# Optimization experiments

Measured on AMD Instinct MI355X. Metric: run time of the kernel, lower is better.

## Reference

```python
import jax, jax.numpy as jnp
import numpy as np

N_NODES = 100000
N_HEDGES = 20000
N_PAIRS = 1600000
D = 128


def setup_inputs() -> dict:
    key = jax.random.key(0)
    k1, k2, k3, k4, k5 = jax.random.split(key, 5)
    features = jax.random.normal(k1, (N_NODES, D), dtype=jnp.float32)
    W = jax.random.normal(k2, (D, D), dtype=jnp.float32) * (1.0 / np.sqrt(D))
    b = jax.random.normal(k3, (D,), dtype=jnp.float32) * 0.01
    node_idx = jax.random.randint(k4, (N_PAIRS,), 0, N_NODES, dtype=jnp.int32)
    hedge_idx = jax.random.randint(k5, (N_PAIRS,), 0, N_HEDGES, dtype=jnp.int32)
    return {"features": features, "W": W, "b": b,
            "node_idx": node_idx, "hedge_idx": hedge_idx, "n_hedges": N_HEDGES}


def reference(features, W, b, node_idx, hedge_idx, n_hedges):
    # features: [N, D]; (node_idx, hedge_idx): [E] incidence pairs
    N = features.shape[0]
    ones = jnp.ones(node_idx.shape, dtype=features.dtype)
    # node -> hyperedge mean (DGL copy_u + mean over 'in' etype)
    deg_e = jax.ops.segment_sum(ones, hedge_idx, num_segments=n_hedges)  # [He]
    h_edge = jax.ops.segment_sum(features[node_idx], hedge_idx, num_segments=n_hedges)
    h_edge = h_edge / jnp.maximum(deg_e, 1.0)[:, None]  # zero-degree edges -> 0
    # hyperedge -> node mean (copy_u + mean over 'contains' etype)
    deg_n = jax.ops.segment_sum(ones, node_idx, num_segments=N)  # [N]
    h_node = jax.ops.segment_sum(h_edge[hedge_idx], node_idx, num_segments=N)
    h_node = h_node / jnp.maximum(deg_n, 1.0)[:, None]
    # nn.Linear: x @ W.T + b
    return h_node @ W.T + b
```

## Files before the change

### kernel.cpp

```cpp
#include <hip/hip_runtime.h>

static constexpr int kD = 128;
static constexpr int kHedges = 20000;

static constexpr int kNCE = 157;
static constexpr int kCapCE = 11264;
static constexpr int kNCN = 196;
static constexpr int kCapCN = 9216;
static constexpr int kSliceE4 = 1664;
static constexpr int kSliceN4 = 1408;
static constexpr int kPmax = 1600;

__device__ __forceinline__ float u2f(unsigned u) { return __uint_as_float(u); }
__device__ __forceinline__ unsigned f2u(float f) { return __float_as_uint(f); }

__device__ __forceinline__ unsigned bfpack(float x, float y) {
  unsigned ux = f2u(x); ux = (ux + 0x7FFFu + ((ux >> 16) & 1u)) >> 16;
  unsigned uy = f2u(y); uy = (uy + 0x7FFFu + ((uy >> 16) & 1u)) & 0xFFFF0000u;
  return ux | uy;
}
__device__ __forceinline__ void bf8_acc(uint4 v, float* a) {
  a[0] += u2f(v.x << 16); a[1] += u2f(v.x & 0xFFFF0000u);
  a[2] += u2f(v.y << 16); a[3] += u2f(v.y & 0xFFFF0000u);
  a[4] += u2f(v.z << 16); a[5] += u2f(v.z & 0xFFFF0000u);
  a[6] += u2f(v.w << 16); a[7] += u2f(v.w & 0xFFFF0000u);
}

__global__ __launch_bounds__(256) void partition_coarse(
    const float* __restrict__ feat, unsigned* __restrict__ feat_bf, int n_feat,
    const float* __restrict__ W, unsigned* __restrict__ Wt2g,
    const int* __restrict__ node_idx, const int* __restrict__ hedge_idx,
    int n_pairs,
    int* __restrict__ gcnt_e, int* __restrict__ buf_e,
    int* __restrict__ gcnt_n, int* __restrict__ buf_n) {
  __shared__ unsigned lbuf_e[kPmax];
  __shared__ unsigned lbuf_n[kPmax];
  __shared__ int he[kNCE], se[kNCE];
  __shared__ int hn[kNCN], sn_[kNCN];
  __shared__ int wtot[4];
  const int tid = threadIdx.x;
  {
    const int n8 = n_feat >> 3;
    for (int t = blockIdx.x * 256 + tid; t < n8; t += gridDim.x * 256) {
      long long i = (long long)t * 8;
      const float4 v0 = *(const float4*)(feat + i);
      const float4 v1 = *(const float4*)(feat + i + 4);
      uint4 o;
      o.x = bfpack(v0.x, v0.y); o.y = bfpack(v0.z, v0.w);
      o.z = bfpack(v1.x, v1.y); o.w = bfpack(v1.z, v1.w);
      *(uint4*)(feat_bf + (i >> 1)) = o;
    }
  }
  for (int t = blockIdx.x * 256 + tid; t < kD * 64; t += gridDim.x * 256) {
    int k = t & 127, j = t >> 7;
    Wt2g[k * 64 + j] = bfpack(W[(2 * j) * kD + k], W[(2 * j + 1) * kD + k]);
  }
  const int per_block = (n_pairs + gridDim.x - 1) / gridDim.x;
  const int s = blockIdx.x * per_block;
  const int e = min(s + per_block, n_pairs);
  const int cnt = max(e - s, 0);
  for (int i = tid; i < kNCE; i += 256) he[i] = 0;
  for (int i = tid; i < kNCN; i += 256) hn[i] = 0;
  __syncthreads();
  for (int i = s + tid; i < e; i += 256) {
    atomicAdd(&he[hedge_idx[i] >> 7], 1);
    atomicAdd(&hn[node_idx[i] >> 9], 1);
  }
  __syncthreads();
  const int lane = tid & 63, wid = tid >> 6;
  {
    int v = (tid < kNCE) ? he[tid] : 0;
    int x = v;
#pragma unroll
    for (int d = 1; d < 64; d <<= 1) {
      int y = __shfl_up(x, d, 64);
      if (lane >= d) x += y;
    }
    if (lane == 63) wtot[wid] = x;
    __syncthreads();
    int add = 0;
    for (int w = 0; w < wid; ++w) add += wtot[w];
    if (tid < kNCE) {
      int lofs = x + add - v;
      int base = (v > 0) ? atomicAdd(&gcnt_e[tid], v) : 0;
      se[tid] = base - lofs;
      he[tid] = lofs;
    }
  }
  __syncthreads();
  {
    int v = (tid < kNCN) ? hn[tid] : 0;
    int x = v;
#pragma unroll
    for (int d = 1; d < 64; d <<= 1) {
      int y = __shfl_up(x, d, 64);
      if (lane >= d) x += y;
    }
    if (lane == 63) wtot[wid] = x;
    __syncthreads();
    int add = 0;
    for (int w = 0; w < wid; ++w) add += wtot[w];
    if (tid < kNCN) {
      int lofs = x + add - v;
      int base = (v > 0) ? atomicAdd(&gcnt_n[tid], v) : 0;
      sn_[tid] = base - lofs;
      hn[tid] = lofs;
    }
  }
  __syncthreads();
  for (int i = s + tid; i < e; i += 256) {
    const unsigned n = (unsigned)node_idx[i];
    const unsigned h = (unsigned)hedge_idx[i];
    const int be = (int)(h >> 7);
    const int p = atomicAdd(&he[be], 1);
    lbuf_e[p] = (n << 15) | h;
    const int bn = (int)(n >> 9);
    const int q = atomicAdd(&hn[bn], 1);
    lbuf_n[q] = (h << 17) | n;
  }
  __syncthreads();
  for (int i = tid; i < cnt; i += 256) {
    const unsigned v = lbuf_e[i];
    const int h = (int)(v & 0x7FFFu);
    const int n = (int)(v >> 15);
    const int b = h >> 7;
    const int pe = se[b] + i;
    if (pe < kCapCE) buf_e[(long long)b * kCapCE + pe] = (n << 7) | (h & 127);
  }
  for (int i = tid; i < cnt; i += 256) {
    const unsigned v = lbuf_n[i];
    const int n = (int)(v & 0x1FFFFu);
    const int h = (int)(v >> 17);
    const int b = n >> 9;
    const int pn = sn_[b] + i;
    if (pn < kCapCN) buf_n[(long long)b * kCapCN + pn] = (h << 9) | (n & 511);
  }
}

__global__ __launch_bounds__(1024) void subsort_kernel(
    int* __restrict__ buf_e, const int* __restrict__ gcnt_e, int* __restrict__ seg_e,
    int* __restrict__ buf_n, const int* __restrict__ gcnt_n, int* __restrict__ seg_n) {
  __shared__ int sbuf[kCapCE];
  __shared__ int bins[513];
  __shared__ int cur[512];
  __shared__ int segs[513];
  __shared__ int wtot[16];
  const int tid = threadIdx.x;
  int nbins, shift, cnt; int* src; int* segout;
  if (blockIdx.x < kNCE) {
    int cb = blockIdx.x; nbins = 128; shift = 7;
    src = buf_e + (long long)cb * kCapCE;
    cnt = min(gcnt_e[cb], kCapCE);
    segout = seg_e + cb * 129;
  } else {
    int cb = blockIdx.x - kNCE; nbins = 512; shift = 9;
    src = buf_n + (long long)cb * kCapCN;
    cnt = min(gcnt_n[cb], kCapCN);
    segout = seg_n + cb * 513;
  }
  const int mask = nbins - 1;
  for (int i = tid; i < nbins; i += 1024) bins[i] = 0;
  __syncthreads();
  for (int i = tid; i < cnt; i += 1024) atomicAdd(&bins[src[i] & mask], 1);
  __syncthreads();
  const int lane = tid & 63, wid = tid >> 6;
  int v = (tid < nbins) ? bins[tid] : 0;
  int x = v;
#pragma unroll
  for (int d = 1; d < 64; d <<= 1) {
    int y = __shfl_up(x, d, 64);
    if (lane >= d) x += y;
  }
  if (lane == 63) wtot[wid] = x;
  __syncthreads();
  int add = 0;
  for (int w = 0; w < wid; ++w) add += wtot[w];
  if (tid < nbins) { segs[tid + 1] = x + add; cur[tid] = x + add - v; }
  if (tid == 0) segs[0] = 0;
  __syncthreads();
  for (int i = tid; i < cnt; i += 1024) {
    int p = src[i];
    int r = atomicAdd(&cur[p & mask], 1);
    sbuf[r] = p >> shift;
  }
  __syncthreads();
  for (int i = tid; i < cnt; i += 1024) src[i] = sbuf[i];
  for (int j = tid; j <= nbins; j += 1024) segout[j] = segs[j];
}

__global__ __launch_bounds__(256) void gather_edge_fused(
    const unsigned* __restrict__ feat_bf, const int* __restrict__ buf_e,
    const int* __restrict__ seg_e, const unsigned* __restrict__ Wt2g,
    unsigned* __restrict__ t_edge, int n_hedges) {
  __shared__ int ebuf[kSliceE4];
  __shared__ int segl[17];
  __shared__ float hrow[16][132];
  const int b = blockIdx.x;
  const int tid = threadIdx.x;
  const int h0 = b * 16;
  const int cb = h0 >> 7, j0 = h0 & 127;
  if (tid < 17) segl[tid] = seg_e[cb * 129 + j0 + tid];
  __syncthreads();
  const int sbase = segl[0];
  const int n_sl = min(segl[16] - sbase, kSliceE4);
  const int* src = buf_e + (long long)cb * kCapCE + sbase;
  for (int i = tid; i < n_sl; i += 256) ebuf[i] = src[i];
  __syncthreads();
  const int g = tid >> 4, lane = tid & 15, cw = lane * 4;
  const int gh = h0 + g;
  float a[8] = {}, a2[8] = {};
  int deg = 0;
  if (gh < n_hedges) {
    deg = segl[g + 1] - segl[g];
    const int s0 = min(segl[g] - sbase, n_sl);
    const int e0 = min(segl[g + 1] - sbase, n_sl);
    int j = s0;
    const int jend8 = s0 + ((e0 - s0) & ~7);
    if (j < jend8) {
      uint4 A0 = *(const uint4*)(feat_bf + (long long)ebuf[j] * 64 + cw);
      uint4 A1 = *(const uint4*)(feat_bf + (long long)ebuf[j + 1] * 64 + cw);
      uint4 A2 = *(const uint4*)(feat_bf + (long long)ebuf[j + 2] * 64 + cw);
      uint4 A3 = *(const uint4*)(feat_bf + (long long)ebuf[j + 3] * 64 + cw);
      uint4 A4 = *(const uint4*)(feat_bf + (long long)ebuf[j + 4] * 64 + cw);
      uint4 A5 = *(const uint4*)(feat_bf + (long long)ebuf[j + 5] * 64 + cw);
      uint4 A6 = *(const uint4*)(feat_bf + (long long)ebuf[j + 6] * 64 + cw);
      uint4 A7 = *(const uint4*)(feat_bf + (long long)ebuf[j + 7] * 64 + cw);
      j += 8;
      for (; j < jend8; j += 8) {
        uint4 B0 = *(const uint4*)(feat_bf + (long long)ebuf[j] * 64 + cw);
        uint4 B1 = *(const uint4*)(feat_bf + (long long)ebuf[j + 1] * 64 + cw);
        uint4 B2 = *(const uint4*)(feat_bf + (long long)ebuf[j + 2] * 64 + cw);
        uint4 B3 = *(const uint4*)(feat_bf + (long long)ebuf[j + 3] * 64 + cw);
        uint4 B4 = *(const uint4*)(feat_bf + (long long)ebuf[j + 4] * 64 + cw);
        uint4 B5 = *(const uint4*)(feat_bf + (long long)ebuf[j + 5] * 64 + cw);
        uint4 B6 = *(const uint4*)(feat_bf + (long long)ebuf[j + 6] * 64 + cw);
        uint4 B7 = *(const uint4*)(feat_bf + (long long)ebuf[j + 7] * 64 + cw);
        bf8_acc(A0, a); bf8_acc(A1, a2); bf8_acc(A2, a); bf8_acc(A3, a2);
        bf8_acc(A4, a); bf8_acc(A5, a2); bf8_acc(A6, a); bf8_acc(A7, a2);
        A0 = B0; A1 = B1; A2 = B2; A3 = B3;
        A4 = B4; A5 = B5; A6 = B6; A7 = B7;
      }
      bf8_acc(A0, a); bf8_acc(A1, a2); bf8_acc(A2, a); bf8_acc(A3, a2);
      bf8_acc(A4, a); bf8_acc(A5, a2); bf8_acc(A6, a); bf8_acc(A7, a2);
    }
    for (; j < e0; ++j) {
      uint4 v = *(const uint4*)(feat_bf + (long long)ebuf[j] * 64 + cw);
      bf8_acc(v, a);
    }
  }
  {
    const float inv = 1.0f / fmaxf((float)deg, 1.0f);
    float4 r0, r1;
    r0.x = (a[0] + a2[0]) * inv; r0.y = (a[1] + a2[1]) * inv;
    r0.z = (a[2] + a2[2]) * inv; r0.w = (a[3] + a2[3]) * inv;
    r1.x = (a[4] + a2[4]) * inv; r1.y = (a[5] + a2[5]) * inv;
    r1.z = (a[6] + a2[6]) * inv; r1.w = (a[7] + a2[7]) * inv;
    *(float4*)(&hrow[g][lane * 8]) = r0;
    *(float4*)(&hrow[g][lane * 8 + 4]) = r1;
  }
  __syncthreads();
  const unsigned* wrow = Wt2g + lane * 4;
  float acc[8] = {};
#pragma unroll 2
  for (int k = 0; k < kD; ++k) {
    const uint4 wp = *(const uint4*)(wrow + k * 64);
    const float hk = hrow[g][k];
    acc[0] = fmaf(hk, u2f(wp.x << 16), acc[0]);
    acc[1] = fmaf(hk, u2f(wp.x & 0xFFFF0000u), acc[1]);
    acc[2] = fmaf(hk, u2f(wp.y << 16), acc[2]);
    acc[3] = fmaf(hk, u2f(wp.y & 0xFFFF0000u), acc[3]);
    acc[4] = fmaf(hk, u2f(wp.z << 16), acc[4]);
    acc[5] = fmaf(hk, u2f(wp.z & 0xFFFF0000u), acc[5]);
    acc[6] = fmaf(hk, u2f(wp.w << 16), acc[6]);
    acc[7] = fmaf(hk, u2f(wp.w & 0xFFFF0000u), acc[7]);
  }
  if (gh < n_hedges) {
    uint4 o;
    o.x = bfpack(acc[0], acc[1]);
    o.y = bfpack(acc[2], acc[3]);
    o.z = bfpack(acc[4], acc[5]);
    o.w = bfpack(acc[6], acc[7]);
    *(uint4*)(t_edge + (long long)gh * 64 + cw) = o;
  }
}

__global__ __launch_bounds__(256) void gather_node_v4(
    const unsigned* __restrict__ t_edge, const int* __restrict__ buf_n,
    const int* __restrict__ seg_n, const float* __restrict__ bias,
    float* __restrict__ out, int n_nodes) {
  __shared__ int ebuf[kSliceN4];
  __shared__ int segl[65];
  const int b = blockIdx.x;
  const int tid = threadIdx.x;
  const int n0 = b * 64;
  const int cb = n0 >> 9, j0 = n0 & 511;
  if (tid < 65) segl[tid] = seg_n[cb * 513 + j0 + tid];
  __syncthreads();
  const int sbase = segl[0];
  const int n_sl = min(segl[64] - sbase, kSliceN4);
  const int* src = buf_n + (long long)cb * kCapCN + sbase;
  for (int i = tid; i < n_sl; i += 256) ebuf[i] = src[i];
  __syncthreads();
  const int g = tid >> 4, lane = tid & 15, cw = lane * 4;
  const float4 b0 = *(const float4*)(bias + lane * 8);
  const float4 b1 = *(const float4*)(bias + lane * 8 + 4);
  for (int nl = g; nl < 64; nl += 16) {
    int gn = n0 + nl;
    if (gn >= n_nodes) continue;
    const int deg = segl[nl + 1] - segl[nl];
    const int s0 = min(segl[nl] - sbase, n_sl);
    const int e0 = min(segl[nl + 1] - sbase, n_sl);
    float a[8] = {}, a2[8] = {};
    int j = s0;
    const int jend8 = s0 + ((e0 - s0) & ~7);
    if (j < jend8) {
      uint4 A0 = *(const uint4*)(t_edge + (long long)ebuf[j] * 64 + cw);
      uint4 A1 = *(const uint4*)(t_edge + (long long)ebuf[j + 1] * 64 + cw);
      uint4 A2 = *(const uint4*)(t_edge + (long long)ebuf[j + 2] * 64 + cw);
      uint4 A3 = *(const uint4*)(t_edge + (long long)ebuf[j + 3] * 64 + cw);
      uint4 A4 = *(const uint4*)(t_edge + (long long)ebuf[j + 4] * 64 + cw);
      uint4 A5 = *(const uint4*)(t_edge + (long long)ebuf[j + 5] * 64 + cw);
      uint4 A6 = *(const uint4*)(t_edge + (long long)ebuf[j + 6] * 64 + cw);
      uint4 A7 = *(const uint4*)(t_edge + (long long)ebuf[j + 7] * 64 + cw);
      j += 8;
      for (; j < jend8; j += 8) {
        uint4 B0 = *(const uint4*)(t_edge + (long long)ebuf[j] * 64 + cw);
        uint4 B1 = *(const uint4*)(t_edge + (long long)ebuf[j + 1] * 64 + cw);
        uint4 B2 = *(const uint4*)(t_edge + (long long)ebuf[j + 2] * 64 + cw);
        uint4 B3 = *(const uint4*)(t_edge + (long long)ebuf[j + 3] * 64 + cw);
        uint4 B4 = *(const uint4*)(t_edge + (long long)ebuf[j + 4] * 64 + cw);
        uint4 B5 = *(const uint4*)(t_edge + (long long)ebuf[j + 5] * 64 + cw);
        uint4 B6 = *(const uint4*)(t_edge + (long long)ebuf[j + 6] * 64 + cw);
        uint4 B7 = *(const uint4*)(t_edge + (long long)ebuf[j + 7] * 64 + cw);
        bf8_acc(A0, a); bf8_acc(A1, a2); bf8_acc(A2, a); bf8_acc(A3, a2);
        bf8_acc(A4, a); bf8_acc(A5, a2); bf8_acc(A6, a); bf8_acc(A7, a2);
        A0 = B0; A1 = B1; A2 = B2; A3 = B3;
        A4 = B4; A5 = B5; A6 = B6; A7 = B7;
      }
      bf8_acc(A0, a); bf8_acc(A1, a2); bf8_acc(A2, a); bf8_acc(A3, a2);
      bf8_acc(A4, a); bf8_acc(A5, a2); bf8_acc(A6, a); bf8_acc(A7, a2);
    }
    for (; j < e0; ++j) {
      uint4 v = *(const uint4*)(t_edge + (long long)ebuf[j] * 64 + cw);
      bf8_acc(v, a);
    }
#pragma unroll
    for (int t = 0; t < 8; ++t) a[t] += a2[t];
    float inv = 1.0f / fmaxf((float)deg, 1.0f);
    float4 o0, o1;
    o0.x = fmaf(a[0], inv, b0.x); o0.y = fmaf(a[1], inv, b0.y);
    o0.z = fmaf(a[2], inv, b0.z); o0.w = fmaf(a[3], inv, b0.w);
    o1.x = fmaf(a[4], inv, b1.x); o1.y = fmaf(a[5], inv, b1.y);
    o1.z = fmaf(a[6], inv, b1.z); o1.w = fmaf(a[7], inv, b1.w);
    float* op = out + (long long)gn * kD + lane * 8;
    *(float4*)op = o0;
    *(float4*)(op + 4) = o1;
  }
}

extern "C" void kernel_launch(void* const* d_in, const int* in_sizes, int n_in,
                              void* d_out, int out_size, void* d_ws, size_t ws_size,
                              hipStream_t stream) {
  const float* feat      = (const float*)d_in[0];
  const float* W         = (const float*)d_in[1];
  const float* b         = (const float*)d_in[2];
  const int*   node_idx  = (const int*)d_in[3];
  const int*   hedge_idx = (const int*)d_in[4];

  const int n_pairs  = in_sizes[3];
  const int n_nodes  = in_sizes[0] / kD;
  const int n_hedges = kHedges;
  const int n_feat   = in_sizes[0];

  unsigned* feat_bf = (unsigned*)d_out;

  const int n_rows_pad = ((n_hedges + 63) / 64) * 64;
  unsigned* t_edge = (unsigned*)d_ws;
  int* buf_e = (int*)(t_edge + (size_t)n_rows_pad * 64);
  int* buf_n = buf_e + (size_t)kNCE * kCapCE;
  int* seg_e = buf_n + (size_t)kNCN * kCapCN;
  int* seg_n = seg_e + (size_t)kNCE * 129;
  int* gcnt_e = seg_n + (size_t)kNCN * 513;
  int* gcnt_n = gcnt_e + kNCE;
  unsigned* Wt2g = (unsigned*)(gcnt_n + kNCN);

  hipMemsetAsync(gcnt_e, 0, (size_t)(kNCE + kNCN) * sizeof(int), stream);

  int pgrid = (n_pairs + kPmax - 1) / kPmax;
  if (pgrid < 512) pgrid = 512;

  partition_coarse<<<pgrid, 256, 0, stream>>>(
      feat, feat_bf, n_feat, W, Wt2g,
      node_idx, hedge_idx, n_pairs, gcnt_e, buf_e, gcnt_n, buf_n);

  subsort_kernel<<<kNCE + kNCN, 1024, 0, stream>>>(
      buf_e, gcnt_e, seg_e, buf_n, gcnt_n, seg_n);

  gather_edge_fused<<<(n_hedges + 15) / 16, 256, 0, stream>>>(
      feat_bf, buf_e, seg_e, Wt2g, t_edge, n_hedges);

  gather_node_v4<<<(n_nodes + 63) / 64, 256, 0, stream>>>(
      t_edge, buf_n, seg_n, b, (float*)d_out, n_nodes);
}
```

Measured before the change: 283.5 us.

## Use bf16 MFMA for the per-hyperedge linear transform and enlarge partition chunk

Replaces the scalar FMA loop that multiplied each 16-row hyperedge tile by W with bf16 MFMA 16x16x32 instructions. The mean rows are packed to bf16 in shared memory, W is stored row-major in bf16, and results are staged through shared memory before being packed to t_edge. This also doubles kPmax, which halves the number of partition blocks and doubles the pairs each block handles. The MFMA path adds a bf16 rounding of the intermediate means and an extra shared-memory round trip.

```diff
diff --git a/kernel.cpp b/kernel.cpp
--- a/kernel.cpp
+++ b/kernel.cpp
@@ -9,7 +9,10 @@
 static constexpr int kCapCN = 9216;
 static constexpr int kSliceE4 = 1664;
 static constexpr int kSliceN4 = 1408;
-static constexpr int kPmax = 1600;
+static constexpr int kPmax = 3200;
+
+typedef __attribute__((ext_vector_type(8))) short bf16x8;
+typedef __attribute__((ext_vector_type(4))) float f32x4;
 
 __device__ __forceinline__ float u2f(unsigned u) { return __uint_as_float(u); }
 __device__ __forceinline__ unsigned f2u(float f) { return __float_as_uint(f); }
@@ -28,7 +31,7 @@
 
 __global__ __launch_bounds__(256) void partition_coarse(
     const float* __restrict__ feat, unsigned* __restrict__ feat_bf, int n_feat,
-    const float* __restrict__ W, unsigned* __restrict__ Wt2g,
+    const float* __restrict__ W, unsigned* __restrict__ Wbf,
     const int* __restrict__ node_idx, const int* __restrict__ hedge_idx,
     int n_pairs,
     int* __restrict__ gcnt_e, int* __restrict__ buf_e,
@@ -52,8 +55,8 @@
     }
   }
   for (int t = blockIdx.x * 256 + tid; t < kD * 64; t += gridDim.x * 256) {
-    int k = t & 127, j = t >> 7;
-    Wt2g[k * 64 + j] = bfpack(W[(2 * j) * kD + k], W[(2 * j + 1) * kD + k]);
+    int row = t >> 6, m = t & 63;
+    Wbf[t] = bfpack(W[row * kD + 2 * m], W[row * kD + 2 * m + 1]);
   }
   const int per_block = (n_pairs + gridDim.x - 1) / gridDim.x;
   const int s = blockIdx.x * per_block;
@@ -190,11 +193,12 @@
 
 __global__ __launch_bounds__(256) void gather_edge_fused(
     const unsigned* __restrict__ feat_bf, const int* __restrict__ buf_e,
-    const int* __restrict__ seg_e, const unsigned* __restrict__ Wt2g,
+    const int* __restrict__ seg_e, const unsigned* __restrict__ Wbf,
     unsigned* __restrict__ t_edge, int n_hedges) {
   __shared__ int ebuf[kSliceE4];
   __shared__ int segl[17];
-  __shared__ float hrow[16][132];
+  __shared__ unsigned hbf[16][68];
+  __shared__ float hout[16][132];
   const int b = blockIdx.x;
   const int tid = threadIdx.x;
   const int h0 = b * 16;
@@ -250,36 +254,43 @@
   }
   {
     const float inv = 1.0f / fmaxf((float)deg, 1.0f);
-    float4 r0, r1;
-    r0.x = (a[0] + a2[0]) * inv; r0.y = (a[1] + a2[1]) * inv;
-    r0.z = (a[2] + a2[2]) * inv; r0.w = (a[3] + a2[3]) * inv;
-    r1.x = (a[4] + a2[4]) * inv; r1.y = (a[5] + a2[5]) * inv;
-    r1.z = (a[6] + a2[6]) * inv; r1.w = (a[7] + a2[7]) * inv;
-    *(float4*)(&hrow[g][lane * 8]) = r0;
-    *(float4*)(&hrow[g][lane * 8 + 4]) = r1;
-  }
-  __syncthreads();
-  const unsigned* wrow = Wt2g + lane * 4;
-  float acc[8] = {};
-#pragma unroll 2
-  for (int k = 0; k < kD; ++k) {
-    const uint4 wp = *(const uint4*)(wrow + k * 64);
-    const float hk = hrow[g][k];
-    acc[0] = fmaf(hk, u2f(wp.x << 16), acc[0]);
-    acc[1] = fmaf(hk, u2f(wp.x & 0xFFFF0000u), acc[1]);
-    acc[2] = fmaf(hk, u2f(wp.y << 16), acc[2]);
-    acc[3] = fmaf(hk, u2f(wp.y & 0xFFFF0000u), acc[3]);
-    acc[4] = fmaf(hk, u2f(wp.z << 16), acc[4]);
-    acc[5] = fmaf(hk, u2f(wp.z & 0xFFFF0000u), acc[5]);
-    acc[6] = fmaf(hk, u2f(wp.w << 16), acc[6]);
-    acc[7] = fmaf(hk, u2f(wp.w & 0xFFFF0000u), acc[7]);
-  }
+    uint4 o;
+    o.x = bfpack((a[0] + a2[0]) * inv, (a[1] + a2[1]) * inv);
+    o.y = bfpack((a[2] + a2[2]) * inv, (a[3] + a2[3]) * inv);
+    o.z = bfpack((a[4] + a2[4]) * inv, (a[5] + a2[5]) * inv);
+    o.w = bfpack((a[6] + a2[6]) * inv, (a[7] + a2[7]) * inv);
+    *(uint4*)(&hbf[g][cw]) = o;
+  }
+  __syncthreads();
+  {
+    const int wv = tid >> 6;
+    const int l = tid & 63;
+    const int frow = l & 15;
+    const int kgrp = l >> 4;
+    f32x4 acc0 = {0.f, 0.f, 0.f, 0.f}, acc1 = {0.f, 0.f, 0.f, 0.f};
+#pragma unroll
+    for (int kk = 0; kk < 4; ++kk) {
+      const int wofs = kk * 16 + kgrp * 4;
+      bf16x8 af = *(const bf16x8*)(&hbf[frow][wofs]);
+      bf16x8 bf0 = *(const bf16x8*)(Wbf + ((2 * wv) * 16 + frow) * 64 + wofs);
+      bf16x8 bf1 = *(const bf16x8*)(Wbf + ((2 * wv + 1) * 16 + frow) * 64 + wofs);
+      acc0 = __builtin_amdgcn_mfma_f32_16x16x32_bf16(af, bf0, acc0, 0, 0, 0);
+      acc1 = __builtin_amdgcn_mfma_f32_16x16x32_bf16(af, bf1, acc1, 0, 0, 0);
+    }
+#pragma unroll
+    for (int r = 0; r < 4; ++r) {
+      hout[kgrp * 4 + r][(2 * wv) * 16 + frow] = acc0[r];
+      hout[kgrp * 4 + r][(2 * wv + 1) * 16 + frow] = acc1[r];
+    }
+  }
+  __syncthreads();
   if (gh < n_hedges) {
+    const float* hr = &hout[g][lane * 8];
     uint4 o;
-    o.x = bfpack(acc[0], acc[1]);
-    o.y = bfpack(acc[2], acc[3]);
-    o.z = bfpack(acc[4], acc[5]);
-    o.w = bfpack(acc[6], acc[7]);
+    o.x = bfpack(hr[0], hr[1]);
+    o.y = bfpack(hr[2], hr[3]);
+    o.z = bfpack(hr[4], hr[5]);
+    o.w = bfpack(hr[6], hr[7]);
     *(uint4*)(t_edge + (long long)gh * 64 + cw) = o;
   }
 }
@@ -382,7 +393,7 @@
   int* seg_n = seg_e + (size_t)kNCE * 129;
   int* gcnt_e = seg_n + (size_t)kNCN * 513;
   int* gcnt_n = gcnt_e + kNCE;
-  unsigned* Wt2g = (unsigned*)(gcnt_n + kNCN);
+  unsigned* Wbf = (unsigned*)(gcnt_n + kNCN);
 
   hipMemsetAsync(gcnt_e, 0, (size_t)(kNCE + kNCN) * sizeof(int), stream);
 
@@ -390,14 +401,14 @@
   if (pgrid < 512) pgrid = 512;
 
   partition_coarse<<<pgrid, 256, 0, stream>>>(
-      feat, feat_bf, n_feat, W, Wt2g,
+      feat, feat_bf, n_feat, W, Wbf,
       node_idx, hedge_idx, n_pairs, gcnt_e, buf_e, gcnt_n, buf_n);
 
   subsort_kernel<<<kNCE + kNCN, 1024, 0, stream>>>(
       buf_e, gcnt_e, seg_e, buf_n, gcnt_n, seg_n);
 
   gather_edge_fused<<<(n_hedges + 15) / 16, 256, 0, stream>>>(
-      feat_bf, buf_e, seg_e, Wt2g, t_edge, n_hedges);
+      feat_bf, buf_e, seg_e, Wbf, t_edge, n_hedges);
 
   gather_node_v4<<<(n_nodes + 63) / 64, 256, 0, stream>>>(
       t_edge, buf_n, seg_n, b, (float*)d_out, n_nodes);
```

Result: faster. 259.3 us (-8.5%).
